# Kernel optimization log

Hardware: AMD Instinct MI355X
Metric: run time of the kernel (lower is better)

## Reference

```python
import jax, jax.numpy as jnp
import numpy as np

N_QUBITS = 12
LAYERS = 3


def _apply(state, mats, axes):
    """Apply batched k-qubit gate. state: [B]+[2]*n complex64; mats: [B, 2^k, 2^k]; axes: state axes (1-based)."""
    k = len(axes)
    d = 2 ** k
    s = jnp.moveaxis(state, axes, tuple(range(1, k + 1)))
    shp = s.shape
    s = jnp.einsum('bij,bjk->bik', mats, s.reshape(shp[0], d, -1))
    return jnp.moveaxis(s.reshape(shp), tuple(range(1, k + 1)), axes)


def _ry(theta):
    # RY(theta) = [[cos(t/2), -sin(t/2)], [sin(t/2), cos(t/2)]], batched over B
    c = jnp.cos(theta / 2).astype(jnp.complex64)
    s = jnp.sin(theta / 2).astype(jnp.complex64)
    return jnp.stack([jnp.stack([c, -s], -1), jnp.stack([s, c], -1)], -2)


def _crx(theta):
    # CRX: identity on control=0 subspace, RX(theta) on control=1 subspace (basis order |ct>)
    c = jnp.cos(theta / 2).astype(jnp.complex64)
    s = (-1j) * jnp.sin(theta / 2).astype(jnp.complex64)
    o = jnp.ones_like(c)
    z = jnp.zeros_like(c)
    rows = [[o, z, z, z], [z, o, z, z], [z, z, c, s], [z, z, s, c]]
    return jnp.stack([jnp.stack(r, -1) for r in rows], -2)


def _circuit(state_re, state_im, params):
    B = params.shape[0]
    n = N_QUBITS
    state = (state_re + 1j * state_im).astype(jnp.complex64).reshape((B,) + (2,) * n)
    p = params.reshape(B, LAYERS, 4, n)  # param idx order: RY block, CRX block, RY block, CRX block
    for l in range(LAYERS):
        th = p[:, l]
        for w in range(n):
            state = _apply(state, _ry(th[:, 0, w]), (w + 1,))
        for i, w in enumerate(reversed(range(n))):
            state = _apply(state, _crx(th[:, 1, i]), (w + 1, ((w + 1) % n) + 1))
        for w in range(n):
            state = _apply(state, _ry(th[:, 2, w]), (w + 1,))
        for i, w in enumerate([n - 1] + list(range(n - 1))):
            state = _apply(state, _crx(th[:, 3, i]), (w + 1, ((w - 1) % n) + 1))
    state = state.reshape(B, -1)
    return jnp.stack([state.real, state.imag], -1)  # [B, 2^n, 2]


def setup_inputs() -> dict:
    key = jax.random.key(0)
    k1, k2, k3 = jax.random.split(key, 3)
    B = 128
    dim = 2 ** N_QUBITS
    return {
        'state_re': jax.random.normal(k1, (B, dim), jnp.float32),
        'state_im': jax.random.normal(k2, (B, dim), jnp.float32),
        'params': jax.random.normal(k3, (B, LAYERS * 4 * N_QUBITS), jnp.float32),
    }


def reference(state_re, state_im, params):
    return _circuit(state_re, state_im, params)
```

## Files before the change

### kernel.cpp

```cpp
#include <hip/hip_runtime.h>
#include <math.h>

#define DIM  4096
#define BLK  512
#define NPAR 144

typedef float v2f __attribute__((ext_vector_type(2)));

struct Ph { int reg[3]; int wav[3]; };
struct TMap { unsigned pk[9]; unsigned short so[8]; unsigned short rn[8]; };

constexpr int REGS[12][3] = {
  {11,0,1},{1,2,3},{3,4,5},{5,6,7},{7,8,9},{9,10,11},
  {11,0,1},{9,10,11},{7,8,9},{5,6,7},{3,4,5},{1,2,3}};

constexpr Ph phaseAt(int i) {
  Ph p = {};
  if (i == 0 || i == 37) {
    p.reg[0]=0; p.reg[1]=1; p.reg[2]=2;
    p.wav[0]=9; p.wav[1]=10; p.wav[2]=11;
    return p;
  }
  int e = (i - 1) % 12;
  for (int j = 0; j < 3; ++j) p.reg[j] = REGS[e][j];
  bool A = (e <= 2) || (e >= 10);
  p.wav[0] = A ? 6 : 2; p.wav[1] = A ? 7 : 3; p.wav[2] = A ? 8 : 4;
  return p;
}
constexpr bool inArr(const int* a, int n, int b) {
  for (int i = 0; i < n; ++i) if (a[i] == b) return true;
  return false;
}
constexpr int idxOf3(const int* a, int v) {
  for (int j = 0; j < 3; ++j) if (a[j] == v) return j;
  return -1;
}
constexpr bool isLoc(int t) {
  if (t == 0 || t == 36) return false;
  Ph a = phaseAt(t), b = phaseAt(t + 1);
  return a.wav[0]==b.wav[0] && a.wav[1]==b.wav[1] && a.wav[2]==b.wav[2];
}
constexpr int bufIdx(int t) {
  int k = 0;
  for (int u = 0; u <= t; ++u) if (!isLoc(u)) ++k;
  return (k + 1) & 1;
}
constexpr int sharedBit(Ph o, Ph n) {
  for (int j = 0; j < 3; ++j) if (inArr(n.reg, 3, o.reg[j])) return o.reg[j];
  return -1;
}

struct BuildOut { TMap m; int js, jn; bool ok; };

constexpr BuildOut buildT(Ph o, Ph n, bool local) {
  BuildOut R = {};
  R.ok = true;
  int s = sharedBit(o, n);
  if (s < 0) { R.ok = false; return R; }
  R.js = idxOf3(o.reg, s);
  R.jn = idxOf3(n.reg, s);
  if (R.js < 0 || R.jn < 0) { R.ok = false; return R; }
  bool lo[12] = {}, ln[12] = {};
  for (int b = 0; b < 12; ++b) {
    lo[b] = !inArr(o.reg,3,b) && !inArr(o.wav,3,b);
    ln[b] = !inArr(n.reg,3,b) && !inArr(n.wav,3,b);
  }
  int col[12] = {};
  bool uo[12] = {}, un[12] = {}, consumed[12] = {};
  col[s] = 1; consumed[s] = true;
  int row = 1;
  for (int b = 0; b < 12 && row < 4; ++b)
    if (lo[b] && ln[b] && !consumed[b]) { col[b] = 1 << row; uo[b]=un[b]=true; consumed[b]=true; ++row; }
  while (row < 4) {
    int a = -1, c = -1;
    for (int b = 0; b < 12; ++b) if (lo[b] && !uo[b] && !consumed[b]) { a = b; break; }
    for (int b = 0; b < 12; ++b) if (ln[b] && !un[b] && !consumed[b] && b != a) { c = b; break; }
    if (a < 0 || c < 0) { R.ok = false; return R; }
    col[a] |= 1 << row; col[c] |= 1 << row;
    uo[a]=true; un[c]=true; consumed[c]=true;
    ++row;
  }
  if (local) {
    for (int i = 0; i < 3; ++i) {
      if (consumed[o.wav[i]]) { R.ok = false; return R; }
      col[o.wav[i]] |= 1 << (9 + i);
      consumed[o.wav[i]] = true;
    }
    int rr = 4;
    for (int b = 0; b < 12; ++b) if (!consumed[b]) { col[b] |= 1 << rr; ++rr; }
    if (rr != 9) { R.ok = false; return R; }
  } else {
    int rr = 4;
    for (int b = 0; b < 12; ++b) if (!consumed[b]) { col[b] |= 1 << rr; ++rr; }
    if (rr != 12) { R.ok = false; return R; }
  }
  {
    int pv[12] = {}, pb[12] = {};
    int nr = 0;
    for (int b = 0; b < 12; ++b) {
      int v = col[b];
      for (int k = 0; k < nr; ++k) if (v & pb[k]) v ^= pv[k];
      if (v) { pb[nr] = v & (-v); pv[nr] = v; ++nr; }
    }
    if (nr != 12) { R.ok = false; return R; }
  }
  int Lo[6] = {}, Ln[6] = {};
  int i0 = 0, i1 = 0;
  for (int b = 0; b < 12; ++b) { if (lo[b]) Lo[i0++] = b; if (ln[b]) Ln[i1++] = b; }
  if (i0 != 6 || i1 != 6) { R.ok = false; return R; }
  for (int i = 0; i < 9; ++i) {
    unsigned po = (i < 6) ? (unsigned)col[Lo[i]] : (unsigned)col[o.wav[i-6]];
    unsigned pn = (i < 6) ? (unsigned)col[Ln[i]] : (unsigned)col[n.wav[i-6]];
    R.m.pk[i] = po | (pn << 16);
  }
  for (int r = 0; r < 8; ++r) {
    int a = 0, c = 0;
    for (int j = 0; j < 3; ++j)
      if ((r >> j) & 1) { a ^= col[o.reg[j]]; c ^= col[n.reg[j]]; }
    R.m.so[r] = (unsigned short)(a * 8);
    R.m.rn[r] = (unsigned short)(c * 8);
  }
  return R;
}

struct AllT { TMap t[37]; bool loc[37]; int buf[37]; int js[37]; int jn[37]; bool ok; };
constexpr AllT buildAll() {
  AllT A = {};
  A.ok = true;
  for (int t = 0; t < 37; ++t) {
    BuildOut b = buildT(phaseAt(t), phaseAt(t + 1), isLoc(t));
    A.t[t] = b.m;
    A.ok = A.ok && b.ok;
    A.loc[t] = isLoc(t);
    A.buf[t] = bufIdx(t);
    A.js[t] = b.js;
    A.jn[t] = b.jn;
  }
  return A;
}
constexpr AllT AT = buildAll();
static_assert(AT.ok, "slot-map construction failed");

__device__ __forceinline__ float rlf(float v, int l) {
  return __int_as_float(__builtin_amdgcn_readlane(__float_as_int(v), l));
}
template<int AO>
__device__ __forceinline__ v2f angAt(const float (&ct)[3], const float (&st)[3]) {
  v2f a;
  a.x = rlf(ct[AO >> 6], AO & 63);
  a.y = rlf(st[AO >> 6], AO & 63);
  return a;
}

template<int J>
__device__ __forceinline__ void ry8(v2f (&z)[8], v2f a) {
  const float c = a.x, s = a.y;
  #pragma unroll
  for (int p = 0; p < 4; ++p) {
    const int r0 = ((p & ~((1 << J) - 1)) << 1) | (p & ((1 << J) - 1));
    const int r1 = r0 | (1 << J);
    v2f u = z[r0], v = z[r1];
    z[r0] = c * u - s * v;
    z[r1] = s * u + c * v;
  }
}
template<int JC, int JT>
__device__ __forceinline__ void crx8(v2f (&z)[8], v2f a) {
  const float c = a.x, s = a.y;
  constexpr int MC = 1 << JC, MT = 1 << JT;
  constexpr int mlo = MC < MT ? MC : MT;
  constexpr int mhi = MC < MT ? MT : MC;
  #pragma unroll
  for (int p = 0; p < 2; ++p) {
    int q = ((p & ~(mlo - 1)) << 1) | (p & (mlo - 1));
    q = ((q & ~(mhi - 1)) << 1) | (q & (mhi - 1));
    const int r0 = q | MC, r1 = r0 | MT;
    v2f u = z[r0], v = z[r1];
    v2f n0, n1;
    n0.x = c * u.x + s * v.y;
    n0.y = c * u.y - s * v.x;
    n1.x = c * v.x + s * u.y;
    n1.y = c * v.y - s * u.x;
    z[r0] = n0; z[r1] = n1;
  }
}

template<int E, int L>
__device__ __forceinline__ void gates(v2f (&z)[8], const float (&ct)[3], const float (&st)[3]) {
#define A(k) (angAt<48 * L + (k)>(ct, st))
  if constexpr (E == 0)      { ry8<0>(z,A(0));  ry8<1>(z,A(11)); ry8<2>(z,A(10));
                               crx8<1,0>(z,A(12)); crx8<2,1>(z,A(13)); }
  else if constexpr (E == 1) { ry8<1>(z,A(9));  ry8<2>(z,A(8));
                               crx8<1,0>(z,A(14)); crx8<2,1>(z,A(15)); }
  else if constexpr (E == 2) { ry8<1>(z,A(7));  ry8<2>(z,A(6));
                               crx8<1,0>(z,A(16)); crx8<2,1>(z,A(17)); }
  else if constexpr (E == 3) { ry8<1>(z,A(5));  ry8<2>(z,A(4));
                               crx8<1,0>(z,A(18)); crx8<2,1>(z,A(19)); }
  else if constexpr (E == 4) { ry8<1>(z,A(3));  ry8<2>(z,A(2));
                               crx8<1,0>(z,A(20)); crx8<2,1>(z,A(21)); }
  else if constexpr (E == 5) { ry8<1>(z,A(1));
                               crx8<1,0>(z,A(22)); crx8<2,1>(z,A(23)); }
  else if constexpr (E == 6) { ry8<0>(z,A(24)); ry8<1>(z,A(35)); ry8<2>(z,A(34));
                               crx8<1,2>(z,A(36)); crx8<0,1>(z,A(37)); }
  else if constexpr (E == 7) { ry8<0>(z,A(26)); ry8<1>(z,A(25));
                               crx8<1,2>(z,A(38)); crx8<0,1>(z,A(39)); }
  else if constexpr (E == 8) { ry8<0>(z,A(28)); ry8<1>(z,A(27));
                               crx8<1,2>(z,A(40)); crx8<0,1>(z,A(41)); }
  else if constexpr (E == 9) { ry8<0>(z,A(30)); ry8<1>(z,A(29));
                               crx8<1,2>(z,A(42)); crx8<0,1>(z,A(43)); }
  else if constexpr (E == 10){ ry8<0>(z,A(32)); ry8<1>(z,A(31));
                               crx8<1,2>(z,A(44)); crx8<0,1>(z,A(45)); }
  else                       { ry8<1>(z,A(33));
                               crx8<1,2>(z,A(46)); crx8<0,1>(z,A(47)); }
#undef A
}

template<int T>
__device__ __forceinline__ void restage(v2f (&z)[8], int tid, char* Lb, char* C0, char* C1) {
  constexpr bool LOC = AT.loc[T];
  constexpr int JS = AT.js[T], JN = AT.jn[T];
  char* buf = LOC ? Lb : (AT.buf[T] ? C1 : C0);
  unsigned acc = 0;
  #pragma unroll
  for (int i = 0; i < 9; ++i)
    acc ^= (unsigned)(-((tid >> i) & 1)) & AT.t[T].pk[i];
  const unsigned bo = (acc & 0xfffu) << 3;
  const unsigned bn = ((acc >> 16) & 0xfffu) << 3;
  #pragma unroll
  for (int r = 0; r < 8; ++r) {
    if (r & (1 << JS)) continue;
    v2f z0 = z[r], z1 = z[r | (1 << JS)];
    float4 w; w.x = z0.x; w.y = z0.y; w.z = z1.x; w.w = z1.y;
    *(float4*)(buf + (bo ^ AT.t[T].so[r])) = w;
  }
  if (LOC) {
    asm volatile("" ::: "memory");
  } else {
    __syncthreads();
  }
  #pragma unroll
  for (int r = 0; r < 8; ++r) {
    if (r & (1 << JN)) continue;
    float4 w = *(const float4*)(buf + (bn ^ AT.t[T].rn[r]));
    v2f z0, z1;
    z0.x = w.x; z0.y = w.y;
    z1.x = w.z; z1.y = w.w;
    z[r] = z0;
    z[r | (1 << JN)] = z1;
  }
}

template<int L>
__device__ __forceinline__ void layer(v2f (&z)[8], int tid,
                                      const float (&ct)[3], const float (&st)[3],
                                      char* Lb, char* C0, char* C1) {
  gates<0, L>(z, ct, st);  restage<12*L + 1>(z, tid, Lb, C0, C1);
  gates<1, L>(z, ct, st);  restage<12*L + 2>(z, tid, Lb, C0, C1);
  gates<2, L>(z, ct, st);  restage<12*L + 3>(z, tid, Lb, C0, C1);
  gates<3, L>(z, ct, st);  restage<12*L + 4>(z, tid, Lb, C0, C1);
  gates<4, L>(z, ct, st);  restage<12*L + 5>(z, tid, Lb, C0, C1);
  gates<5, L>(z, ct, st);  restage<12*L + 6>(z, tid, Lb, C0, C1);
  gates<6, L>(z, ct, st);  restage<12*L + 7>(z, tid, Lb, C0, C1);
  gates<7, L>(z, ct, st);  restage<12*L + 8>(z, tid, Lb, C0, C1);
  gates<8, L>(z, ct, st);  restage<12*L + 9>(z, tid, Lb, C0, C1);
  gates<9, L>(z, ct, st);  restage<12*L + 10>(z, tid, Lb, C0, C1);
  gates<10, L>(z, ct, st); restage<12*L + 11>(z, tid, Lb, C0, C1);
  gates<11, L>(z, ct, st);
  if constexpr (L < 2) restage<12*L + 12>(z, tid, Lb, C0, C1);
}

__global__ __launch_bounds__(BLK) void ansatz_kernel(
    const float* __restrict__ sre, const float* __restrict__ sim,
    const float* __restrict__ params, float* __restrict__ out) {

  __shared__ alignas(16) v2f C0s[DIM], C1s[DIM], Ls[DIM];

  const int b = blockIdx.x, tid = threadIdx.x;
  char* C0 = (char*)C0s;
  char* C1 = (char*)C1s;
  char* Lb = (char*)Ls;

  float ct[3], st[3];
  {
    const int lane = tid & 63;
    #pragma unroll
    for (int j = 0; j < 3; ++j) {
      int idx = lane + 64 * j;
      int ci = (idx < NPAR) ? idx : 0;
      float th = params[(size_t)b * NPAR + ci];
      sincosf(0.5f * th, &st[j], &ct[j]);
    }
  }

  v2f z[8];
  {
    int base = ((tid & 15) << 2) | ((tid & 16) << 5) | ((tid & 32) << 5)
             | (tid & 64) | (tid & 128) | (tid & 256);
    const float4* pr = (const float4*)(sre + (size_t)b * DIM + base);
    const float4* pi = (const float4*)(sim + (size_t)b * DIM + base);
    float4 f0 = pr[0], f1 = pr[512];
    float4 g0 = pi[0], g1 = pi[512];
    z[0].x = f0.x; z[0].y = g0.x;  z[2].x = f0.y; z[2].y = g0.y;
    z[4].x = f0.z; z[4].y = g0.z;  z[6].x = f0.w; z[6].y = g0.w;
    z[1].x = f1.x; z[1].y = g1.x;  z[3].x = f1.y; z[3].y = g1.y;
    z[5].x = f1.z; z[5].y = g1.z;  z[7].x = f1.w; z[7].y = g1.w;
  }

  layer<0>(z, tid, ct, st, Lb, C0, C1);
  layer<1>(z, tid, ct, st, Lb, C0, C1);
  layer<2>(z, tid, ct, st, Lb, C0, C1);

  {
    int base = (tid & 1) | ((tid & 2) << 3) | ((tid & 4) << 3)
             | ((tid & 8) << 6) | ((tid & 16) << 6) | ((tid & 32) << 6)
             | (tid & 64) | (tid & 128) | (tid & 256);
    v2f* o2 = (v2f*)out + (size_t)b * DIM + base;
    #pragma unroll
    for (int r = 0; r < 8; ++r)
      o2[2 * r] = z[r];
  }
}

extern "C" void kernel_launch(void* const* d_in, const int* in_sizes, int n_in,
                              void* d_out, int out_size, void* d_ws, size_t ws_size,
                              hipStream_t stream) {
  const float* sre    = (const float*)d_in[0];
  const float* sim    = (const float*)d_in[1];
  const float* params = (const float*)d_in[2];
  float* out          = (float*)d_out;

  const int B = in_sizes[0] / DIM;
  ansatz_kernel<<<B, BLK, 0, stream>>>(sre, sim, params, out);
}
```

Baseline: 78.54 us.

## Hold 16 amplitudes per thread with 4-qubit register phases, 256-thread blocks

Each thread now keeps 16 amplitudes in registers (4 register qubits, 2 wave qubits) instead of 8, and blocks shrink from 512 to 256 threads. This cuts the restage phases per layer from 12 to 8 and the block-wide syncs to 6 in total, so less LDS shuffling and fewer barriers are needed. The per-thread shuffle offsets are precomputed once into arrays instead of being rebuilt every phase. The cost is higher register pressure, and with only 128 blocks of 256 threads there is less parallelism per CU.

```diff
diff --git a/kernel.cpp b/kernel.cpp
--- a/kernel.cpp
+++ b/kernel.cpp
@@ -2,43 +2,38 @@
 #include <math.h>
 
 #define DIM  4096
-#define BLK  512
+#define BLK  256
 #define NPAR 144
 
 typedef float v2f __attribute__((ext_vector_type(2)));
 
-struct Ph { int reg[3]; int wav[3]; };
-struct TMap { unsigned pk[9]; unsigned short so[8]; unsigned short rn[8]; };
-
-constexpr int REGS[12][3] = {
-  {11,0,1},{1,2,3},{3,4,5},{5,6,7},{7,8,9},{9,10,11},
-  {11,0,1},{9,10,11},{7,8,9},{5,6,7},{3,4,5},{1,2,3}};
+struct Ph { int reg[4]; int wav[2]; };
+struct TMap { unsigned pk[8]; unsigned short so[16]; unsigned short rn[16]; };
+
+constexpr int REGS4[8][4] = {
+  {11,0,1,2},{2,3,4,5},{5,6,7,8},{8,9,10,11},
+  {10,11,0,1},{7,8,9,10},{4,5,6,7},{1,2,3,4}};
+constexpr int PINS[8][2] = {
+  {9,10},{9,10},{9,10},{2,3},{2,3},{2,3},{2,3},{9,10}};
 
 constexpr Ph phaseAt(int i) {
   Ph p = {};
-  if (i == 0 || i == 37) {
-    p.reg[0]=0; p.reg[1]=1; p.reg[2]=2;
-    p.wav[0]=9; p.wav[1]=10; p.wav[2]=11;
-    return p;
-  }
-  int e = (i - 1) % 12;
-  for (int j = 0; j < 3; ++j) p.reg[j] = REGS[e][j];
-  bool A = (e <= 2) || (e >= 10);
-  p.wav[0] = A ? 6 : 2; p.wav[1] = A ? 7 : 3; p.wav[2] = A ? 8 : 4;
+  int e = (i == 0) ? 0 : (i - 1) % 8;
+  for (int j = 0; j < 4; ++j) p.reg[j] = REGS4[e][j];
+  p.wav[0] = PINS[e][0]; p.wav[1] = PINS[e][1];
   return p;
 }
 constexpr bool inArr(const int* a, int n, int b) {
   for (int i = 0; i < n; ++i) if (a[i] == b) return true;
   return false;
 }
-constexpr int idxOf3(const int* a, int v) {
-  for (int j = 0; j < 3; ++j) if (a[j] == v) return j;
+constexpr int idxOf4(const int* a, int v) {
+  for (int j = 0; j < 4; ++j) if (a[j] == v) return j;
   return -1;
 }
 constexpr bool isLoc(int t) {
-  if (t == 0 || t == 36) return false;
   Ph a = phaseAt(t), b = phaseAt(t + 1);
-  return a.wav[0]==b.wav[0] && a.wav[1]==b.wav[1] && a.wav[2]==b.wav[2];
+  return a.wav[0]==b.wav[0] && a.wav[1]==b.wav[1];
 }
 constexpr int bufIdx(int t) {
   int k = 0;
@@ -46,7 +41,7 @@
   return (k + 1) & 1;
 }
 constexpr int sharedBit(Ph o, Ph n) {
-  for (int j = 0; j < 3; ++j) if (inArr(n.reg, 3, o.reg[j])) return o.reg[j];
+  for (int j = 0; j < 4; ++j) if (inArr(n.reg, 4, o.reg[j])) return o.reg[j];
   return -1;
 }
 
@@ -57,13 +52,13 @@
   R.ok = true;
   int s = sharedBit(o, n);
   if (s < 0) { R.ok = false; return R; }
-  R.js = idxOf3(o.reg, s);
-  R.jn = idxOf3(n.reg, s);
+  R.js = idxOf4(o.reg, s);
+  R.jn = idxOf4(n.reg, s);
   if (R.js < 0 || R.jn < 0) { R.ok = false; return R; }
   bool lo[12] = {}, ln[12] = {};
   for (int b = 0; b < 12; ++b) {
-    lo[b] = !inArr(o.reg,3,b) && !inArr(o.wav,3,b);
-    ln[b] = !inArr(n.reg,3,b) && !inArr(n.wav,3,b);
+    lo[b] = !inArr(o.reg,4,b) && !inArr(o.wav,2,b);
+    ln[b] = !inArr(n.reg,4,b) && !inArr(n.wav,2,b);
   }
   int col[12] = {};
   bool uo[12] = {}, un[12] = {}, consumed[12] = {};
@@ -81,14 +76,14 @@
     ++row;
   }
   if (local) {
-    for (int i = 0; i < 3; ++i) {
+    for (int i = 0; i < 2; ++i) {
       if (consumed[o.wav[i]]) { R.ok = false; return R; }
-      col[o.wav[i]] |= 1 << (9 + i);
+      col[o.wav[i]] |= 1 << (10 + i);
       consumed[o.wav[i]] = true;
     }
     int rr = 4;
     for (int b = 0; b < 12; ++b) if (!consumed[b]) { col[b] |= 1 << rr; ++rr; }
-    if (rr != 9) { R.ok = false; return R; }
+    if (rr != 10) { R.ok = false; return R; }
   } else {
     int rr = 4;
     for (int b = 0; b < 12; ++b) if (!consumed[b]) { col[b] |= 1 << rr; ++rr; }
@@ -104,18 +99,18 @@
     }
     if (nr != 12) { R.ok = false; return R; }
   }
-  int Lo[6] = {}, Ln[6] = {};
+  int Lo[6] = {}, Ln6[6] = {};
   int i0 = 0, i1 = 0;
-  for (int b = 0; b < 12; ++b) { if (lo[b]) Lo[i0++] = b; if (ln[b]) Ln[i1++] = b; }
+  for (int b = 0; b < 12; ++b) { if (lo[b]) Lo[i0++] = b; if (ln[b]) Ln6[i1++] = b; }
   if (i0 != 6 || i1 != 6) { R.ok = false; return R; }
-  for (int i = 0; i < 9; ++i) {
+  for (int i = 0; i < 8; ++i) {
     unsigned po = (i < 6) ? (unsigned)col[Lo[i]] : (unsigned)col[o.wav[i-6]];
-    unsigned pn = (i < 6) ? (unsigned)col[Ln[i]] : (unsigned)col[n.wav[i-6]];
+    unsigned pn = (i < 6) ? (unsigned)col[Ln6[i]] : (unsigned)col[n.wav[i-6]];
     R.m.pk[i] = po | (pn << 16);
   }
-  for (int r = 0; r < 8; ++r) {
+  for (int r = 0; r < 16; ++r) {
     int a = 0, c = 0;
-    for (int j = 0; j < 3; ++j)
+    for (int j = 0; j < 4; ++j)
       if ((r >> j) & 1) { a ^= col[o.reg[j]]; c ^= col[n.reg[j]]; }
     R.m.so[r] = (unsigned short)(a * 8);
     R.m.rn[r] = (unsigned short)(c * 8);
@@ -123,11 +118,18 @@
   return R;
 }
 
-struct AllT { TMap t[37]; bool loc[37]; int buf[37]; int js[37]; int jn[37]; bool ok; };
+constexpr bool mapsEqual(const TMap& a, const TMap& b) {
+  for (int i = 0; i < 8; ++i) if (a.pk[i] != b.pk[i]) return false;
+  for (int r = 0; r < 16; ++r)
+    if (a.so[r] != b.so[r] || a.rn[r] != b.rn[r]) return false;
+  return true;
+}
+
+struct AllT { TMap t[24]; bool loc[24]; int buf[24]; int js[24]; int jn[24]; bool ok; };
 constexpr AllT buildAll() {
   AllT A = {};
   A.ok = true;
-  for (int t = 0; t < 37; ++t) {
+  for (int t = 0; t < 24; ++t) {
     BuildOut b = buildT(phaseAt(t), phaseAt(t + 1), isLoc(t));
     A.t[t] = b.m;
     A.ok = A.ok && b.ok;
@@ -136,6 +138,18 @@
     A.js[t] = b.js;
     A.jn[t] = b.jn;
   }
+  for (int t = 9; t < 24; ++t)
+    A.ok = A.ok && mapsEqual(A.t[t], A.t[t-8]) && A.loc[t] == A.loc[t-8]
+         && A.buf[t] == A.buf[t-8] && A.js[t] == A.js[t-8] && A.jn[t] == A.jn[t-8];
+  {
+    int ng = 0;
+    for (int t = 1; t < 24; ++t) if (!A.loc[t]) ++ng;
+    A.ok = A.ok && (ng == 6);
+    for (int t = 1; t < 24; ++t) {
+      bool expectGlob = (((t - 1) % 8) == 2) || (((t - 1) % 8) == 6);
+      A.ok = A.ok && (A.loc[t] == !expectGlob);
+    }
+  }
   return A;
 }
 constexpr AllT AT = buildAll();
@@ -153,10 +167,10 @@
 }
 
 template<int J>
-__device__ __forceinline__ void ry8(v2f (&z)[8], v2f a) {
+__device__ __forceinline__ void ry16(v2f (&z)[16], v2f a) {
   const float c = a.x, s = a.y;
   #pragma unroll
-  for (int p = 0; p < 4; ++p) {
+  for (int p = 0; p < 8; ++p) {
     const int r0 = ((p & ~((1 << J) - 1)) << 1) | (p & ((1 << J) - 1));
     const int r1 = r0 | (1 << J);
     v2f u = z[r0], v = z[r1];
@@ -165,13 +179,13 @@
   }
 }
 template<int JC, int JT>
-__device__ __forceinline__ void crx8(v2f (&z)[8], v2f a) {
+__device__ __forceinline__ void crx16(v2f (&z)[16], v2f a) {
   const float c = a.x, s = a.y;
   constexpr int MC = 1 << JC, MT = 1 << JT;
   constexpr int mlo = MC < MT ? MC : MT;
   constexpr int mhi = MC < MT ? MT : MC;
   #pragma unroll
-  for (int p = 0; p < 2; ++p) {
+  for (int p = 0; p < 4; ++p) {
     int q = ((p & ~(mlo - 1)) << 1) | (p & (mlo - 1));
     q = ((q & ~(mhi - 1)) << 1) | (q & (mhi - 1));
     const int r0 = q | MC, r1 = r0 | MT;
@@ -186,52 +200,42 @@
 }
 
 template<int E, int L>
-__device__ __forceinline__ void gates(v2f (&z)[8], const float (&ct)[3], const float (&st)[3]) {
+__device__ __forceinline__ void gates(v2f (&z)[16], const float (&ct)[3], const float (&st)[3]) {
 #define A(k) (angAt<48 * L + (k)>(ct, st))
-  if constexpr (E == 0)      { ry8<0>(z,A(0));  ry8<1>(z,A(11)); ry8<2>(z,A(10));
-                               crx8<1,0>(z,A(12)); crx8<2,1>(z,A(13)); }
-  else if constexpr (E == 1) { ry8<1>(z,A(9));  ry8<2>(z,A(8));
-                               crx8<1,0>(z,A(14)); crx8<2,1>(z,A(15)); }
-  else if constexpr (E == 2) { ry8<1>(z,A(7));  ry8<2>(z,A(6));
-                               crx8<1,0>(z,A(16)); crx8<2,1>(z,A(17)); }
-  else if constexpr (E == 3) { ry8<1>(z,A(5));  ry8<2>(z,A(4));
-                               crx8<1,0>(z,A(18)); crx8<2,1>(z,A(19)); }
-  else if constexpr (E == 4) { ry8<1>(z,A(3));  ry8<2>(z,A(2));
-                               crx8<1,0>(z,A(20)); crx8<2,1>(z,A(21)); }
-  else if constexpr (E == 5) { ry8<1>(z,A(1));
-                               crx8<1,0>(z,A(22)); crx8<2,1>(z,A(23)); }
-  else if constexpr (E == 6) { ry8<0>(z,A(24)); ry8<1>(z,A(35)); ry8<2>(z,A(34));
-                               crx8<1,2>(z,A(36)); crx8<0,1>(z,A(37)); }
-  else if constexpr (E == 7) { ry8<0>(z,A(26)); ry8<1>(z,A(25));
-                               crx8<1,2>(z,A(38)); crx8<0,1>(z,A(39)); }
-  else if constexpr (E == 8) { ry8<0>(z,A(28)); ry8<1>(z,A(27));
-                               crx8<1,2>(z,A(40)); crx8<0,1>(z,A(41)); }
-  else if constexpr (E == 9) { ry8<0>(z,A(30)); ry8<1>(z,A(29));
-                               crx8<1,2>(z,A(42)); crx8<0,1>(z,A(43)); }
-  else if constexpr (E == 10){ ry8<0>(z,A(32)); ry8<1>(z,A(31));
-                               crx8<1,2>(z,A(44)); crx8<0,1>(z,A(45)); }
-  else                       { ry8<1>(z,A(33));
-                               crx8<1,2>(z,A(46)); crx8<0,1>(z,A(47)); }
+  if constexpr (E == 0)      { ry16<0>(z,A(0));  ry16<1>(z,A(11)); ry16<2>(z,A(10)); ry16<3>(z,A(9));
+                               crx16<1,0>(z,A(12)); crx16<2,1>(z,A(13)); crx16<3,2>(z,A(14)); }
+  else if constexpr (E == 1) { ry16<1>(z,A(8));  ry16<2>(z,A(7));  ry16<3>(z,A(6));
+                               crx16<1,0>(z,A(15)); crx16<2,1>(z,A(16)); crx16<3,2>(z,A(17)); }
+  else if constexpr (E == 2) { ry16<1>(z,A(5));  ry16<2>(z,A(4));  ry16<3>(z,A(3));
+                               crx16<1,0>(z,A(18)); crx16<2,1>(z,A(19)); crx16<3,2>(z,A(20)); }
+  else if constexpr (E == 3) { ry16<1>(z,A(2));  ry16<2>(z,A(1));
+                               crx16<1,0>(z,A(21)); crx16<2,1>(z,A(22)); crx16<3,2>(z,A(23)); }
+  else if constexpr (E == 4) { ry16<0>(z,A(25)); ry16<1>(z,A(24)); ry16<2>(z,A(35)); ry16<3>(z,A(34));
+                               crx16<2,3>(z,A(36)); crx16<1,2>(z,A(37)); crx16<0,1>(z,A(38)); }
+  else if constexpr (E == 5) { ry16<0>(z,A(28)); ry16<1>(z,A(27)); ry16<2>(z,A(26));
+                               crx16<2,3>(z,A(39)); crx16<1,2>(z,A(40)); crx16<0,1>(z,A(41)); }
+  else if constexpr (E == 6) { ry16<0>(z,A(31)); ry16<1>(z,A(30)); ry16<2>(z,A(29));
+                               crx16<2,3>(z,A(42)); crx16<1,2>(z,A(43)); crx16<0,1>(z,A(44)); }
+  else                       { ry16<1>(z,A(33)); ry16<2>(z,A(32));
+                               crx16<2,3>(z,A(45)); crx16<1,2>(z,A(46)); crx16<0,1>(z,A(47)); }
 #undef A
 }
 
 template<int T>
-__device__ __forceinline__ void restage(v2f (&z)[8], int tid, char* Lb, char* C0, char* C1) {
+__device__ __forceinline__ void restage(v2f (&z)[16],
+                                        const unsigned (&bo)[8], const unsigned (&bn)[8],
+                                        char* Lb, char* C0, char* C1) {
+  constexpr int K = (T - 1) & 7;
   constexpr bool LOC = AT.loc[T];
   constexpr int JS = AT.js[T], JN = AT.jn[T];
   char* buf = LOC ? Lb : (AT.buf[T] ? C1 : C0);
-  unsigned acc = 0;
-  #pragma unroll
-  for (int i = 0; i < 9; ++i)
-    acc ^= (unsigned)(-((tid >> i) & 1)) & AT.t[T].pk[i];
-  const unsigned bo = (acc & 0xfffu) << 3;
-  const unsigned bn = ((acc >> 16) & 0xfffu) << 3;
-  #pragma unroll
-  for (int r = 0; r < 8; ++r) {
+  const unsigned o = bo[K], n_ = bn[K];
+  #pragma unroll
+  for (int r = 0; r < 16; ++r) {
     if (r & (1 << JS)) continue;
     v2f z0 = z[r], z1 = z[r | (1 << JS)];
     float4 w; w.x = z0.x; w.y = z0.y; w.z = z1.x; w.w = z1.y;
-    *(float4*)(buf + (bo ^ AT.t[T].so[r])) = w;
+    *(float4*)(buf + (o ^ AT.t[T].so[r])) = w;
   }
   if (LOC) {
     asm volatile("" ::: "memory");
@@ -239,9 +243,9 @@
     __syncthreads();
   }
   #pragma unroll
-  for (int r = 0; r < 8; ++r) {
+  for (int r = 0; r < 16; ++r) {
     if (r & (1 << JN)) continue;
-    float4 w = *(const float4*)(buf + (bn ^ AT.t[T].rn[r]));
+    float4 w = *(const float4*)(buf + (n_ ^ AT.t[T].rn[r]));
     v2f z0, z1;
     z0.x = w.x; z0.y = w.y;
     z1.x = w.z; z1.y = w.w;
@@ -251,22 +255,19 @@
 }
 
 template<int L>
-__device__ __forceinline__ void layer(v2f (&z)[8], int tid,
+__device__ __forceinline__ void layer(v2f (&z)[16],
+                                      const unsigned (&bo)[8], const unsigned (&bn)[8],
                                       const float (&ct)[3], const float (&st)[3],
                                       char* Lb, char* C0, char* C1) {
-  gates<0, L>(z, ct, st);  restage<12*L + 1>(z, tid, Lb, C0, C1);
-  gates<1, L>(z, ct, st);  restage<12*L + 2>(z, tid, Lb, C0, C1);
-  gates<2, L>(z, ct, st);  restage<12*L + 3>(z, tid, Lb, C0, C1);
-  gates<3, L>(z, ct, st);  restage<12*L + 4>(z, tid, Lb, C0, C1);
-  gates<4, L>(z, ct, st);  restage<12*L + 5>(z, tid, Lb, C0, C1);
-  gates<5, L>(z, ct, st);  restage<12*L + 6>(z, tid, Lb, C0, C1);
-  gates<6, L>(z, ct, st);  restage<12*L + 7>(z, tid, Lb, C0, C1);
-  gates<7, L>(z, ct, st);  restage<12*L + 8>(z, tid, Lb, C0, C1);
-  gates<8, L>(z, ct, st);  restage<12*L + 9>(z, tid, Lb, C0, C1);
-  gates<9, L>(z, ct, st);  restage<12*L + 10>(z, tid, Lb, C0, C1);
-  gates<10, L>(z, ct, st); restage<12*L + 11>(z, tid, Lb, C0, C1);
-  gates<11, L>(z, ct, st);
-  if constexpr (L < 2) restage<12*L + 12>(z, tid, Lb, C0, C1);
+  gates<0, L>(z, ct, st);  restage<8*L + 1>(z, bo, bn, Lb, C0, C1);
+  gates<1, L>(z, ct, st);  restage<8*L + 2>(z, bo, bn, Lb, C0, C1);
+  gates<2, L>(z, ct, st);  restage<8*L + 3>(z, bo, bn, Lb, C0, C1);
+  gates<3, L>(z, ct, st);  restage<8*L + 4>(z, bo, bn, Lb, C0, C1);
+  gates<4, L>(z, ct, st);  restage<8*L + 5>(z, bo, bn, Lb, C0, C1);
+  gates<5, L>(z, ct, st);  restage<8*L + 6>(z, bo, bn, Lb, C0, C1);
+  gates<6, L>(z, ct, st);  restage<8*L + 7>(z, bo, bn, Lb, C0, C1);
+  gates<7, L>(z, ct, st);
+  if constexpr (L < 2) restage<8*L + 8>(z, bo, bn, Lb, C0, C1);
 }
 
 __global__ __launch_bounds__(BLK) void ansatz_kernel(
@@ -292,31 +293,44 @@
     }
   }
 
-  v2f z[8];
-  {
-    int base = ((tid & 15) << 2) | ((tid & 16) << 5) | ((tid & 32) << 5)
-             | (tid & 64) | (tid & 128) | (tid & 256);
-    const float4* pr = (const float4*)(sre + (size_t)b * DIM + base);
-    const float4* pi = (const float4*)(sim + (size_t)b * DIM + base);
-    float4 f0 = pr[0], f1 = pr[512];
-    float4 g0 = pi[0], g1 = pi[512];
-    z[0].x = f0.x; z[0].y = g0.x;  z[2].x = f0.y; z[2].y = g0.y;
-    z[4].x = f0.z; z[4].y = g0.z;  z[6].x = f0.w; z[6].y = g0.w;
-    z[1].x = f1.x; z[1].y = g1.x;  z[3].x = f1.y; z[3].y = g1.y;
-    z[5].x = f1.z; z[5].y = g1.z;  z[7].x = f1.w; z[7].y = g1.w;
-  }
-
-  layer<0>(z, tid, ct, st, Lb, C0, C1);
-  layer<1>(z, tid, ct, st, Lb, C0, C1);
-  layer<2>(z, tid, ct, st, Lb, C0, C1);
-
-  {
-    int base = (tid & 1) | ((tid & 2) << 3) | ((tid & 4) << 3)
-             | ((tid & 8) << 6) | ((tid & 16) << 6) | ((tid & 32) << 6)
-             | (tid & 64) | (tid & 128) | (tid & 256);
+  unsigned bo[8], bn[8];
+  #pragma unroll
+  for (int k = 0; k < 8; ++k) {
+    unsigned acc = 0;
+    #pragma unroll
+    for (int i = 0; i < 8; ++i)
+      acc ^= (unsigned)(-((tid >> i) & 1)) & AT.t[k + 1].pk[i];
+    bo[k] = (acc & 0xfffu) << 3;
+    bn[k] = ((acc >> 16) & 0xfffu) << 3;
+  }
+
+  v2f z[16];
+  {
+    const float4* pr = (const float4*)(sre + (size_t)b * DIM + (size_t)tid * 8);
+    const float4* pi = (const float4*)(sim + (size_t)b * DIM + (size_t)tid * 8);
+    float4 f0 = pr[0], f1 = pr[1], f2 = pr[512], f3 = pr[513];
+    float4 g0 = pi[0], g1 = pi[1], g2 = pi[512], g3 = pi[513];
+    z[0].x  = f0.x; z[0].y  = g0.x;  z[2].x  = f0.y; z[2].y  = g0.y;
+    z[4].x  = f0.z; z[4].y  = g0.z;  z[6].x  = f0.w; z[6].y  = g0.w;
+    z[8].x  = f1.x; z[8].y  = g1.x;  z[10].x = f1.y; z[10].y = g1.y;
+    z[12].x = f1.z; z[12].y = g1.z;  z[14].x = f1.w; z[14].y = g1.w;
+    z[1].x  = f2.x; z[1].y  = g2.x;  z[3].x  = f2.y; z[3].y  = g2.y;
+    z[5].x  = f2.z; z[5].y  = g2.z;  z[7].x  = f2.w; z[7].y  = g2.w;
+    z[9].x  = f3.x; z[9].y  = g3.x;  z[11].x = f3.y; z[11].y = g3.y;
+    z[13].x = f3.z; z[13].y = g3.z;  z[15].x = f3.w; z[15].y = g3.w;
+  }
+
+  layer<0>(z, bo, bn, ct, st, Lb, C0, C1);
+  layer<1>(z, bo, bn, ct, st, Lb, C0, C1);
+  layer<2>(z, bo, bn, ct, st, Lb, C0, C1);
+
+  {
+    int base = (tid & 1) | ((tid & 2) << 4) | ((tid & 4) << 4)
+             | ((tid & 8) << 4) | ((tid & 16) << 4) | ((tid & 32) << 6)
+             | ((tid & 64) << 3) | ((tid & 128) << 3);
     v2f* o2 = (v2f*)out + (size_t)b * DIM + base;
     #pragma unroll
-    for (int r = 0; r < 8; ++r)
+    for (int r = 0; r < 16; ++r)
       o2[2 * r] = z[r];
   }
 }
```

Measured after the change: 81.70 us. 1.04x slower.

## Replace intra-wave LDS restaging with cross-lane butterfly swaps via DPP and swizzle

Applied to the files above, without the earlier changes.

Intra-wavefront qubit remaps previously round-tripped the state through a third LDS buffer. They now exchange register pairs between lanes with DPP, ds_swizzle or shfl_xor butterflies, followed by a compile-time register permutation. The lane-to-qubit mapping is tracked across transitions at compile time, and a static check confirms the final output layout. This removes LDS traffic and one buffer, but costs extra select instructions and cross-lane ops per butterfly.

```diff
diff --git a/kernel.cpp b/kernel.cpp
--- a/kernel.cpp
+++ b/kernel.cpp
@@ -7,139 +7,176 @@
 
 typedef float v2f __attribute__((ext_vector_type(2)));
 
-struct Ph { int reg[3]; int wav[3]; };
-struct TMap { unsigned pk[9]; unsigned short so[8]; unsigned short rn[8]; };
 
 constexpr int REGS[12][3] = {
   {11,0,1},{1,2,3},{3,4,5},{5,6,7},{7,8,9},{9,10,11},
   {11,0,1},{9,10,11},{7,8,9},{5,6,7},{3,4,5},{1,2,3}};
-
-constexpr Ph phaseAt(int i) {
-  Ph p = {};
-  if (i == 0 || i == 37) {
-    p.reg[0]=0; p.reg[1]=1; p.reg[2]=2;
-    p.wav[0]=9; p.wav[1]=10; p.wav[2]=11;
-    return p;
-  }
-  int e = (i - 1) % 12;
-  for (int j = 0; j < 3; ++j) p.reg[j] = REGS[e][j];
-  bool A = (e <= 2) || (e >= 10);
-  p.wav[0] = A ? 6 : 2; p.wav[1] = A ? 7 : 3; p.wav[2] = A ? 8 : 4;
-  return p;
-}
-constexpr bool inArr(const int* a, int n, int b) {
-  for (int i = 0; i < n; ++i) if (a[i] == b) return true;
-  return false;
-}
-constexpr int idxOf3(const int* a, int v) {
-  for (int j = 0; j < 3; ++j) if (a[j] == v) return j;
-  return -1;
-}
-constexpr bool isLoc(int t) {
-  if (t == 0 || t == 36) return false;
-  Ph a = phaseAt(t), b = phaseAt(t + 1);
-  return a.wav[0]==b.wav[0] && a.wav[1]==b.wav[1] && a.wav[2]==b.wav[2];
-}
-constexpr int bufIdx(int t) {
-  int k = 0;
-  for (int u = 0; u <= t; ++u) if (!isLoc(u)) ++k;
-  return (k + 1) & 1;
-}
-constexpr int sharedBit(Ph o, Ph n) {
-  for (int j = 0; j < 3; ++j) if (inArr(n.reg, 3, o.reg[j])) return o.reg[j];
-  return -1;
-}
-
-struct BuildOut { TMap m; int js, jn; bool ok; };
-
-constexpr BuildOut buildT(Ph o, Ph n, bool local) {
-  BuildOut R = {};
-  R.ok = true;
-  int s = sharedBit(o, n);
-  if (s < 0) { R.ok = false; return R; }
-  R.js = idxOf3(o.reg, s);
-  R.jn = idxOf3(n.reg, s);
-  if (R.js < 0 || R.jn < 0) { R.ok = false; return R; }
-  bool lo[12] = {}, ln[12] = {};
-  for (int b = 0; b < 12; ++b) {
-    lo[b] = !inArr(o.reg,3,b) && !inArr(o.wav,3,b);
-    ln[b] = !inArr(n.reg,3,b) && !inArr(n.wav,3,b);
-  }
-  int col[12] = {};
-  bool uo[12] = {}, un[12] = {}, consumed[12] = {};
-  col[s] = 1; consumed[s] = true;
-  int row = 1;
-  for (int b = 0; b < 12 && row < 4; ++b)
-    if (lo[b] && ln[b] && !consumed[b]) { col[b] = 1 << row; uo[b]=un[b]=true; consumed[b]=true; ++row; }
-  while (row < 4) {
-    int a = -1, c = -1;
-    for (int b = 0; b < 12; ++b) if (lo[b] && !uo[b] && !consumed[b]) { a = b; break; }
-    for (int b = 0; b < 12; ++b) if (ln[b] && !un[b] && !consumed[b] && b != a) { c = b; break; }
-    if (a < 0 || c < 0) { R.ok = false; return R; }
-    col[a] |= 1 << row; col[c] |= 1 << row;
-    uo[a]=true; un[c]=true; consumed[c]=true;
-    ++row;
-  }
-  if (local) {
-    for (int i = 0; i < 3; ++i) {
-      if (consumed[o.wav[i]]) { R.ok = false; return R; }
-      col[o.wav[i]] |= 1 << (9 + i);
-      consumed[o.wav[i]] = true;
-    }
-    int rr = 4;
-    for (int b = 0; b < 12; ++b) if (!consumed[b]) { col[b] |= 1 << rr; ++rr; }
-    if (rr != 9) { R.ok = false; return R; }
-  } else {
-    int rr = 4;
-    for (int b = 0; b < 12; ++b) if (!consumed[b]) { col[b] |= 1 << rr; ++rr; }
-    if (rr != 12) { R.ok = false; return R; }
-  }
-  {
-    int pv[12] = {}, pb[12] = {};
-    int nr = 0;
-    for (int b = 0; b < 12; ++b) {
-      int v = col[b];
-      for (int k = 0; k < nr; ++k) if (v & pb[k]) v ^= pv[k];
-      if (v) { pb[nr] = v & (-v); pv[nr] = v; ++nr; }
-    }
-    if (nr != 12) { R.ok = false; return R; }
-  }
-  int Lo[6] = {}, Ln[6] = {};
-  int i0 = 0, i1 = 0;
-  for (int b = 0; b < 12; ++b) { if (lo[b]) Lo[i0++] = b; if (ln[b]) Ln[i1++] = b; }
-  if (i0 != 6 || i1 != 6) { R.ok = false; return R; }
-  for (int i = 0; i < 9; ++i) {
-    unsigned po = (i < 6) ? (unsigned)col[Lo[i]] : (unsigned)col[o.wav[i-6]];
-    unsigned pn = (i < 6) ? (unsigned)col[Ln[i]] : (unsigned)col[n.wav[i-6]];
-    R.m.pk[i] = po | (pn << 16);
-  }
-  for (int r = 0; r < 8; ++r) {
-    int a = 0, c = 0;
-    for (int j = 0; j < 3; ++j)
-      if ((r >> j) & 1) { a ^= col[o.reg[j]]; c ^= col[n.reg[j]]; }
-    R.m.so[r] = (unsigned short)(a * 8);
-    R.m.rn[r] = (unsigned short)(c * 8);
-  }
-  return R;
-}
-
-struct AllT { TMap t[37]; bool loc[37]; int buf[37]; int js[37]; int jn[37]; bool ok; };
+constexpr bool grpA(int e){ return e<=2 || e>=10; }
+constexpr int wavBit(int e, int i){ return (grpA(e)?6:2)+i; }
+
+constexpr bool inArr(const int* a, int n, int b){
+  for (int i=0;i<n;++i) if (a[i]==b) return true; return false; }
+constexpr int idxOf3(const int* a, int v){
+  for (int j=0;j<3;++j) if (a[j]==v) return j; return -1; }
+
+struct Lam { int p[6]; };
+
+struct Trans {
+  bool loc;
+  int j1,k1,j2,k2;
+  int src[8];
+  unsigned pk[9];
+  unsigned short so[8], rn[8];
+  int js, jn, buf;
+};
+
+struct AllT { Trans t[36]; bool ok; int fin[6]; };
+
 constexpr AllT buildAll() {
   AllT A = {};
   A.ok = true;
-  for (int t = 0; t < 37; ++t) {
-    BuildOut b = buildT(phaseAt(t), phaseAt(t + 1), isLoc(t));
-    A.t[t] = b.m;
-    A.ok = A.ok && b.ok;
-    A.loc[t] = isLoc(t);
-    A.buf[t] = bufIdx(t);
-    A.js[t] = b.js;
-    A.jn[t] = b.jn;
-  }
+  Lam lam = { {2,3,4,5,9,10} };
+  int gcnt = 0;
+  for (int T = 1; T <= 35; ++T) {
+    int e0 = (T-1)%12, e1 = T%12;
+    Trans& t = A.t[T];
+    bool glob = (e1==3 || e1==10);
+    t.loc = !glob;
+    if (glob) {
+      Lam lo = lam;
+      Lam ln = {};
+      {
+        int idx=0;
+        for (int b=0;b<12;++b) {
+          bool used = inArr(REGS[e1],3,b)
+                   || (b>=wavBit(e1,0) && b<=wavBit(e1,2));
+          if (!used) { if (idx<6) ln.p[idx]=b; ++idx; }
+        }
+        if (idx!=6) { A.ok=false; return A; }
+      }
+      int s = -1;
+      for (int j=0;j<3;++j) if (inArr(REGS[e1],3,REGS[e0][j])) s = REGS[e0][j];
+      if (s<0) { A.ok=false; return A; }
+      t.js = idxOf3(REGS[e0], s);
+      t.jn = idxOf3(REGS[e1], s);
+      bool lo_[12]={}, ln_[12]={};
+      for (int b=0;b<12;++b){
+        lo_[b] = inArr(lo.p,6,b);
+        ln_[b] = inArr(ln.p,6,b);
+      }
+      int col[12]={};
+      bool uo[12]={}, un[12]={}, consumed[12]={};
+      col[s]=1; consumed[s]=true;
+      int row=1;
+      for (int b=0;b<12 && row<4;++b)
+        if (lo_[b]&&ln_[b]&&!consumed[b]) {
+          col[b]=1<<row; uo[b]=un[b]=true; consumed[b]=true; ++row;
+        }
+      while (row<4) {
+        int a=-1,c=-1;
+        for (int b=0;b<12;++b) if (lo_[b]&&!uo[b]&&!consumed[b]) { a=b; break; }
+        for (int b=0;b<12;++b) if (ln_[b]&&!un[b]&&!consumed[b]&&b!=a) { c=b; break; }
+        if (a<0||c<0) { A.ok=false; return A; }
+        col[a]|=1<<row; col[c]|=1<<row;
+        uo[a]=true; un[c]=true; consumed[c]=true;
+        ++row;
+      }
+      int rr=4;
+      for (int b=0;b<12;++b) if (!consumed[b]) { col[b]|=1<<rr; ++rr; }
+      if (rr!=12) { A.ok=false; return A; }
+      {
+        int pv[12]={}, pb[12]={}; int nr=0;
+        for (int b=0;b<12;++b){
+          int v=col[b];
+          for (int k=0;k<nr;++k) if (v&pb[k]) v^=pv[k];
+          if (v){ pb[nr]=v&(-v); pv[nr]=v; ++nr; }
+        }
+        if (nr!=12) { A.ok=false; return A; }
+      }
+      for (int i=0;i<9;++i){
+        unsigned po = (i<6)?(unsigned)col[lo.p[i]]:(unsigned)col[wavBit(e0,i-6)];
+        unsigned pn = (i<6)?(unsigned)col[ln.p[i]]:(unsigned)col[wavBit(e1,i-6)];
+        t.pk[i] = po | (pn<<16);
+      }
+      for (int r=0;r<8;++r){
+        int a2=0,c2=0;
+        for (int j=0;j<3;++j) if ((r>>j)&1){ a2^=col[REGS[e0][j]]; c2^=col[REGS[e1][j]]; }
+        t.so[r]=(unsigned short)(a2*8);
+        t.rn[r]=(unsigned short)(c2*8);
+      }
+      t.buf = (++gcnt)&1;
+      lam = ln;
+    } else {
+      if (wavBit(e0,0)!=wavBit(e1,0)) { A.ok=false; return A; }
+      int js_[2]={}, ob[2]={}; int no=0;
+      for (int j=0;j<3;++j)
+        if (!inArr(REGS[e1],3,REGS[e0][j])) {
+          if (no<2){ js_[no]=j; ob[no]=REGS[e0][j]; } ++no;
+        }
+      int ks_[2]={}, ib[2]={}; int ni=0;
+      for (int k=0;k<6;++k)
+        if (inArr(REGS[e1],3,lam.p[k]) && !inArr(REGS[e0],3,lam.p[k])) {
+          if (ni<2){ ks_[ni]=k; ib[ni]=lam.p[k]; } ++ni;
+        }
+      if (no!=2 || ni!=2) { A.ok=false; return A; }
+      t.j1=js_[0]; t.k1=ks_[0]; t.j2=js_[1]; t.k2=ks_[1];
+      int cur[3] = { REGS[e0][0], REGS[e0][1], REGS[e0][2] };
+      cur[js_[0]] = ib[0]; cur[js_[1]] = ib[1];
+      int srcSlot[3] = {};
+      for (int j=0;j<3;++j) {
+        int ss = idxOf3(cur, REGS[e1][j]);
+        if (ss<0) { A.ok=false; return A; }
+        srcSlot[j]=ss;
+      }
+      for (int r=0;r<8;++r){
+        int v=0;
+        for (int j=0;j<3;++j) if ((r>>j)&1) v |= 1<<srcSlot[j];
+        t.src[r]=v;
+      }
+      lam.p[ks_[0]] = ob[0]; lam.p[ks_[1]] = ob[1];
+    }
+  }
+  for (int i=0;i<6;++i) A.fin[i]=lam.p[i];
   return A;
 }
 constexpr AllT AT = buildAll();
-static_assert(AT.ok, "slot-map construction failed");
+static_assert(AT.ok, "transition construction failed");
+static_assert(AT.fin[0]==0 && AT.fin[1]==4 && AT.fin[2]==5 &&
+              AT.fin[3]==9 && AT.fin[4]==10 && AT.fin[5]==11,
+              "final lane layout mismatch");
+
+template<int K>
+__device__ __forceinline__ float lxor(float x) {
+  if constexpr (K == 0) {
+    return __int_as_float(
+      __builtin_amdgcn_mov_dpp(__float_as_int(x), 0xB1, 0xF, 0xF, false));
+  } else if constexpr (K == 1) {
+    return __int_as_float(
+      __builtin_amdgcn_mov_dpp(__float_as_int(x), 0x4E, 0xF, 0xF, false));
+  } else if constexpr (K < 5) {
+    constexpr int imm = ((1 << K) << 10) | 0x1F;
+    return __int_as_float(
+      __builtin_amdgcn_ds_swizzle(__float_as_int(x), imm));
+  } else {
+    return __shfl_xor(x, 32, 64);
+  }
+}
+
+template<int J, int K>
+__device__ __forceinline__ void bfly(v2f (&z)[8], int tid) {
+  const bool q = ((tid >> K) & 1) != 0;
+  #pragma unroll
+  for (int p = 0; p < 4; ++p) {
+    const int r0 = ((p & ~((1 << J) - 1)) << 1) | (p & ((1 << J) - 1));
+    const int r1 = r0 | (1 << J);
+    v2f x = q ? z[r0] : z[r1];
+    v2f xp;
+    xp.x = lxor<K>(x.x);
+    xp.y = lxor<K>(x.y);
+    z[r0] = q ? xp : z[r0];
+    z[r1] = q ? z[r1] : xp;
+  }
+}
 
 __device__ __forceinline__ float rlf(float v, int l) {
   return __int_as_float(__builtin_amdgcn_readlane(__float_as_int(v), l));
@@ -216,69 +253,71 @@
 }
 
 template<int T>
-__device__ __forceinline__ void restage(v2f (&z)[8], int tid, char* Lb, char* C0, char* C1) {
-  constexpr bool LOC = AT.loc[T];
-  constexpr int JS = AT.js[T], JN = AT.jn[T];
-  char* buf = LOC ? Lb : (AT.buf[T] ? C1 : C0);
-  unsigned acc = 0;
-  #pragma unroll
-  for (int i = 0; i < 9; ++i)
-    acc ^= (unsigned)(-((tid >> i) & 1)) & AT.t[T].pk[i];
-  const unsigned bo = (acc & 0xfffu) << 3;
-  const unsigned bn = ((acc >> 16) & 0xfffu) << 3;
-  #pragma unroll
-  for (int r = 0; r < 8; ++r) {
-    if (r & (1 << JS)) continue;
-    v2f z0 = z[r], z1 = z[r | (1 << JS)];
-    float4 w; w.x = z0.x; w.y = z0.y; w.z = z1.x; w.w = z1.y;
-    *(float4*)(buf + (bo ^ AT.t[T].so[r])) = w;
-  }
-  if (LOC) {
-    asm volatile("" ::: "memory");
+__device__ __forceinline__ void trans(v2f (&z)[8], int tid, char* C0, char* C1) {
+  if constexpr (AT.t[T].loc) {
+    bfly<AT.t[T].j1, AT.t[T].k1>(z, tid);
+    bfly<AT.t[T].j2, AT.t[T].k2>(z, tid);
+    v2f tmp[8];
+    #pragma unroll
+    for (int r = 0; r < 8; ++r) tmp[r] = z[r];
+    #pragma unroll
+    for (int r = 0; r < 8; ++r) z[r] = tmp[AT.t[T].src[r]];
   } else {
+    constexpr int JS = AT.t[T].js, JN = AT.t[T].jn;
+    char* buf = AT.t[T].buf ? C1 : C0;
+    unsigned acc = 0;
+    #pragma unroll
+    for (int i = 0; i < 9; ++i)
+      acc ^= (unsigned)(-((tid >> i) & 1)) & AT.t[T].pk[i];
+    const unsigned bo = (acc & 0xfffu) << 3;
+    const unsigned bn = ((acc >> 16) & 0xfffu) << 3;
+    #pragma unroll
+    for (int r = 0; r < 8; ++r) {
+      if (r & (1 << JS)) continue;
+      v2f z0 = z[r], z1 = z[r | (1 << JS)];
+      float4 w; w.x = z0.x; w.y = z0.y; w.z = z1.x; w.w = z1.y;
+      *(float4*)(buf + (bo ^ AT.t[T].so[r])) = w;
+    }
     __syncthreads();
-  }
-  #pragma unroll
-  for (int r = 0; r < 8; ++r) {
-    if (r & (1 << JN)) continue;
-    float4 w = *(const float4*)(buf + (bn ^ AT.t[T].rn[r]));
-    v2f z0, z1;
-    z0.x = w.x; z0.y = w.y;
-    z1.x = w.z; z1.y = w.w;
-    z[r] = z0;
-    z[r | (1 << JN)] = z1;
+    #pragma unroll
+    for (int r = 0; r < 8; ++r) {
+      if (r & (1 << JN)) continue;
+      float4 w = *(const float4*)(buf + (bn ^ AT.t[T].rn[r]));
+      z[r].x = w.x; z[r].y = w.y;
+      z[r | (1 << JN)].x = w.z;
+      z[r | (1 << JN)].y = w.w;
+    }
   }
 }
 
 template<int L>
 __device__ __forceinline__ void layer(v2f (&z)[8], int tid,
                                       const float (&ct)[3], const float (&st)[3],
-                                      char* Lb, char* C0, char* C1) {
-  gates<0, L>(z, ct, st);  restage<12*L + 1>(z, tid, Lb, C0, C1);
-  gates<1, L>(z, ct, st);  restage<12*L + 2>(z, tid, Lb, C0, C1);
-  gates<2, L>(z, ct, st);  restage<12*L + 3>(z, tid, Lb, C0, C1);
-  gates<3, L>(z, ct, st);  restage<12*L + 4>(z, tid, Lb, C0, C1);
-  gates<4, L>(z, ct, st);  restage<12*L + 5>(z, tid, Lb, C0, C1);
-  gates<5, L>(z, ct, st);  restage<12*L + 6>(z, tid, Lb, C0, C1);
-  gates<6, L>(z, ct, st);  restage<12*L + 7>(z, tid, Lb, C0, C1);
-  gates<7, L>(z, ct, st);  restage<12*L + 8>(z, tid, Lb, C0, C1);
-  gates<8, L>(z, ct, st);  restage<12*L + 9>(z, tid, Lb, C0, C1);
-  gates<9, L>(z, ct, st);  restage<12*L + 10>(z, tid, Lb, C0, C1);
-  gates<10, L>(z, ct, st); restage<12*L + 11>(z, tid, Lb, C0, C1);
+                                      char* C0, char* C1) {
+  gates<0, L>(z, ct, st);  trans<12*L + 1>(z, tid, C0, C1);
+  gates<1, L>(z, ct, st);  trans<12*L + 2>(z, tid, C0, C1);
+  gates<2, L>(z, ct, st);  trans<12*L + 3>(z, tid, C0, C1);
+  gates<3, L>(z, ct, st);  trans<12*L + 4>(z, tid, C0, C1);
+  gates<4, L>(z, ct, st);  trans<12*L + 5>(z, tid, C0, C1);
+  gates<5, L>(z, ct, st);  trans<12*L + 6>(z, tid, C0, C1);
+  gates<6, L>(z, ct, st);  trans<12*L + 7>(z, tid, C0, C1);
+  gates<7, L>(z, ct, st);  trans<12*L + 8>(z, tid, C0, C1);
+  gates<8, L>(z, ct, st);  trans<12*L + 9>(z, tid, C0, C1);
+  gates<9, L>(z, ct, st);  trans<12*L + 10>(z, tid, C0, C1);
+  gates<10, L>(z, ct, st); trans<12*L + 11>(z, tid, C0, C1);
   gates<11, L>(z, ct, st);
-  if constexpr (L < 2) restage<12*L + 12>(z, tid, Lb, C0, C1);
+  if constexpr (L < 2) trans<12*L + 12>(z, tid, C0, C1);
 }
 
 __global__ __launch_bounds__(BLK) void ansatz_kernel(
     const float* __restrict__ sre, const float* __restrict__ sim,
     const float* __restrict__ params, float* __restrict__ out) {
 
-  __shared__ alignas(16) v2f C0s[DIM], C1s[DIM], Ls[DIM];
+  __shared__ alignas(16) v2f C0s[DIM], C1s[DIM];
 
   const int b = blockIdx.x, tid = threadIdx.x;
   char* C0 = (char*)C0s;
   char* C1 = (char*)C1s;
-  char* Lb = (char*)Ls;
 
   float ct[3], st[3];
   {
@@ -306,9 +345,9 @@
     z[5].x = f1.z; z[5].y = g1.z;  z[7].x = f1.w; z[7].y = g1.w;
   }
 
-  layer<0>(z, tid, ct, st, Lb, C0, C1);
-  layer<1>(z, tid, ct, st, Lb, C0, C1);
-  layer<2>(z, tid, ct, st, Lb, C0, C1);
+  layer<0>(z, tid, ct, st, C0, C1);
+  layer<1>(z, tid, ct, st, C0, C1);
+  layer<2>(z, tid, ct, st, C0, C1);
 
   {
     int base = (tid & 1) | ((tid & 2) << 3) | ((tid & 4) << 3)
```

Measured after the change: 131.6 us. 1.68x slower.
